# Optimization experiments

Hardware: AMD Instinct MI355X
Metric: run time of the kernel (lower is better)

The kernel has to match this reference:

```python
import jax, jax.numpy as jnp
import numpy as np

TAU = 0.5  # temperature from init_kwargs


def _semi_loss(h1, h2):
    # GRACE-style InfoNCE: -log( e^{sim(i,i')/tau} / (sum_refl + sum_between - e^{sim(i,i)/tau}) )
    n1 = h1 / jnp.linalg.norm(h1, axis=1, keepdims=True)
    n2 = h2 / jnp.linalg.norm(h2, axis=1, keepdims=True)
    refl = jnp.exp((n1 @ n1.T) / TAU)   # [N, N]
    betw = jnp.exp((n1 @ n2.T) / TAU)   # [N, N]
    denom = refl.sum(axis=1) + betw.sum(axis=1) - jnp.diagonal(refl)
    return -jnp.log(jnp.diagonal(betw) / denom)


def _contrast(h1, h2):
    # forward_v1 with batch_size=0 (batched path is mathematically identical)
    return (0.5 * (_semi_loss(h1, h2) + _semi_loss(h2, h1))).mean()


def _proj(z, Wa, ba, Wb, bb):
    # fc_b(elu(fc_a(z))); torch Linear: y = x @ W.T + b
    return jax.nn.elu(z @ Wa.T + ba) @ Wb.T + bb


def setup_inputs() -> dict:
    key = jax.random.key(0)
    ks = jax.random.split(key, 11)
    N, A, B = 8192, 32, 32
    D = A * B
    s = 1.0 / np.sqrt(D)
    inp = {
        'ta': jax.random.normal(ks[0], (N, A, B), dtype=jnp.float32),
        'tb': jax.random.normal(ks[1], (N, A, B), dtype=jnp.float32),
        'W1': jax.random.uniform(ks[2], (D, D), jnp.float32, -s, s),
        'b1': jax.random.uniform(ks[3], (D,), jnp.float32, -s, s),
        'W2': jax.random.uniform(ks[4], (D, D), jnp.float32, -s, s),
        'b2': jax.random.uniform(ks[5], (D,), jnp.float32, -s, s),
        'W3': jax.random.uniform(ks[6], (D, D), jnp.float32, -s, s),
        'b3': jax.random.uniform(ks[7], (D,), jnp.float32, -s, s),
        'W4': jax.random.uniform(ks[8], (D, D), jnp.float32, -s, s),
        'b4': jax.random.uniform(ks[9], (D,), jnp.float32, -s, s),
        'w_r1': jnp.array([0.5], dtype=jnp.float32),
    }
    return inp


def reference(ta, tb, W1, b1, W2, b2, W3, b3, W4, b4, w_r1):
    N = ta.shape[0]
    # row view: [N, A*B]
    z1 = ta.reshape(N, -1)
    z2 = tb.reshape(N, -1)
    loss_row = _contrast(_proj(z1, W1, b1, W2, b2), _proj(z2, W1, b1, W2, b2))
    # column view: permute(0,2,1) then flatten -> [N, B*A]
    z1c = jnp.transpose(ta, (0, 2, 1)).reshape(N, -1)
    z2c = jnp.transpose(tb, (0, 2, 1)).reshape(N, -1)
    loss_col = _contrast(_proj(z1c, W3, b3, W4, b4), _proj(z2c, W3, b3, W4, b4))
    w_row = jnp.clip(w_r1[0], 0.0, 1.0)
    return w_row * loss_row + (1.0 - w_row) * loss_col
```

## Files before the change

kernel.cpp:

```cpp
#include <hip/hip_runtime.h>
#include <stdint.h>


typedef unsigned short u16;
typedef __attribute__((ext_vector_type(8))) __bf16 bf16x8;
typedef __attribute__((ext_vector_type(4))) float f32x4;

#define NS 8192
#define DD 1024

__device__ __forceinline__ float bf2f(u16 u) {
    union { uint32_t i; float f; } v; v.i = ((uint32_t)u) << 16; return v.f;
}
__device__ __forceinline__ u16 f2bf(float f) {
    union { float f; uint32_t i; } v; v.f = f;
    return (u16)((v.i + 0x7FFFu + ((v.i >> 16) & 1u)) >> 16);
}

__device__ __forceinline__ void gload16(const u16* g, u16* l) {
    __builtin_amdgcn_global_load_lds(
        (__attribute__((address_space(1))) void*)(uintptr_t)(g),
        (__attribute__((address_space(3))) void*)(uintptr_t)(l), 16, 0, 0);
}


__global__ __launch_bounds__(256) void conv_f2bf(const float* __restrict__ src,
                                                 u16* __restrict__ dst) {
    int i = (blockIdx.x * 256 + threadIdx.x) * 4;
    float4 v = *(const float4*)(src + i);
    ushort4 o;
    o.x = f2bf(v.x); o.y = f2bf(v.y); o.z = f2bf(v.z); o.w = f2bf(v.w);
    *(ushort4*)(dst + i) = o;
}

__global__ __launch_bounds__(256) void conv_cat(const float* __restrict__ a,
                                                const float* __restrict__ b,
                                                u16* __restrict__ Z) {
    size_t i = (size_t)(blockIdx.x * 256 + threadIdx.x) * 4;
    const size_t half = (size_t)NS * DD;
    const float* s = (i < half) ? (a + i) : (b + (i - half));
    float4 v = *(const float4*)s;
    ushort4 o;
    o.x = f2bf(v.x); o.y = f2bf(v.y); o.z = f2bf(v.z); o.w = f2bf(v.w);
    *(ushort4*)(Z + i) = o;
}

__global__ __launch_bounds__(256) void conv_col(const float* __restrict__ a,
                                                const float* __restrict__ b,
                                                u16* __restrict__ Z) {
    size_t i = (size_t)(blockIdx.x * 256 + threadIdx.x) * 4;
    const size_t half = (size_t)NS * DD;
    const float* src; size_t o;
    if (i < half) { src = a; o = i; } else { src = b; o = i - half; }
    size_t row = o >> 10;
    int j = (int)(o & 1023);
    int aI = j & 31, bI = j >> 5;
    const float* rp = src + (row << 10);
    ushort4 ov;
    ov.x = f2bf(rp[aI * 32 + bI]);
    ov.y = f2bf(rp[(aI + 1) * 32 + bI]);
    ov.z = f2bf(rp[(aI + 2) * 32 + bI]);
    ov.w = f2bf(rp[(aI + 3) * 32 + bI]);
    *(ushort4*)(Z + i) = ov;
}

template <int MODE>
__global__ __launch_bounds__(256) void gemm_bt(const u16* A, const u16* B,
                                               const float* __restrict__ bias,
                                               u16* __restrict__ out) {
    __shared__ alignas(16) u16 As[128 * 32];
    __shared__ alignas(16) u16 Bs[128 * 32];
    const int tid = threadIdx.x;

    const int tm = blockIdx.y, tn = blockIdx.x;
    const size_t tileM = (size_t)tm * 128;
    const size_t tileN = (size_t)tn * 128;

    const int csw = ((tid & 3) ^ ((tid >> 4) & 3)) * 8;
    const u16* gA0 = A + (tileM + (tid >> 2)) * DD + csw;
    const u16* gA1 = gA0 + (size_t)64 * DD;
    const u16* gB0 = B + (tileN + (tid >> 2)) * DD + csw;
    const u16* gB1 = gB0 + (size_t)64 * DD;
    u16* lA0 = &As[tid * 8]; u16* lA1 = lA0 + 2048;
    u16* lB0 = &Bs[tid * 8]; u16* lB1 = lB0 + 2048;

    const int lane = tid & 63;
    const int wv = tid >> 6;
    const int wr = (wv >> 1) << 6;
    const int wc = (wv & 1) << 6;
    const int lr = lane & 15;
    const int lh = lane >> 4;
    const int sw = lh ^ ((lr >> 2) & 3);

    const u16* aBase = &As[(wr + lr) * 32 + sw * 8];
    const u16* bBase = &Bs[(wc + lr) * 32 + sw * 8];

    f32x4 acc[4][4];
#pragma unroll
    for (int i = 0; i < 4; i++)
#pragma unroll
        for (int j = 0; j < 4; j++) acc[i][j] = (f32x4)0.0f;

    for (int k0 = 0; k0 < DD; k0 += 32) {
        gload16(gA0 + k0, lA0);
        gload16(gA1 + k0, lA1);
        gload16(gB0 + k0, lB0);
        gload16(gB1 + k0, lB1);
        __syncthreads();
        bf16x8 af[4], bfr[4];
#pragma unroll
        for (int rt = 0; rt < 4; rt++) af[rt] = *(const bf16x8*)(aBase + rt * 512);
#pragma unroll
        for (int ct = 0; ct < 4; ct++) bfr[ct] = *(const bf16x8*)(bBase + ct * 512);
#pragma unroll
        for (int rt = 0; rt < 4; rt++)
#pragma unroll
            for (int ct = 0; ct < 4; ct++)
                acc[rt][ct] = __builtin_amdgcn_mfma_f32_16x16x32_bf16(
                    af[rt], bfr[ct], acc[rt][ct], 0, 0, 0);
        __syncthreads();
    }

    float bcol[4];
#pragma unroll
    for (int ct = 0; ct < 4; ct++) bcol[ct] = bias[tileN + wc + ct * 16 + lr];
#pragma unroll
    for (int rt = 0; rt < 4; rt++) {
#pragma unroll
        for (int r = 0; r < 4; r++) {
            size_t row = tileM + wr + rt * 16 + lh * 4 + r;
            u16* orow = out + row * DD + tileN + wc + lr;
#pragma unroll
            for (int ct = 0; ct < 4; ct++) {
                float v = acc[rt][ct][r] + bcol[ct];
                if (MODE == 0) v = v > 0.0f ? v : expm1f(v);
                orow[ct * 16] = f2bf(v);
            }
        }
    }
}

__global__ __launch_bounds__(512, 2) void gram256(const u16* __restrict__ H,
                                                  float* __restrict__ S) {
    __shared__ alignas(16) u16 LA[4][256 * 32];
    __shared__ alignas(16) u16 LB[4][256 * 32];
    const int tid = threadIdx.x;

    int x = blockIdx.x, y = blockIdx.y;
    int tm, tn;
    if (y + x < 64) { tm = y;      tn = y + x; }
    else            { tm = 63 - y; tn = x - 1; }

    const size_t rowA = (size_t)tm * 256;
    const size_t rowB = (size_t)tn * 256;

    const int r_lo = tid >> 2;
    const int csw  = ((tid & 3) ^ ((r_lo >> 2) & 3)) * 8;
    const u16* gA0 = H + (rowA + r_lo) * DD + csw;
    const u16* gA1 = H + (rowA + 128 + r_lo) * DD + csw;
    const u16* gB0 = H + (rowB + r_lo) * DD + csw;
    const u16* gB1 = H + (rowB + 128 + r_lo) * DD + csw;
    const int ldst = tid * 8;

    const int lane = tid & 63;
    const int wv = tid >> 6;
    const int wr = (wv >> 2) * 128;
    const int wc = (wv & 3) * 64;
    const int lr = lane & 15;
    const int lh = lane >> 4;
    const int sw = lh ^ ((lr >> 2) & 3);
    const int aoff = (wr + lr) * 32 + sw * 8;
    const int boff = (wc + lr) * 32 + sw * 8;

    f32x4 acc[8][4];
#pragma unroll
    for (int i = 0; i < 8; ++i)
#pragma unroll
        for (int j = 0; j < 4; ++j) acc[i][j] = (f32x4)0.0f;

#pragma unroll
    for (int t = 0; t < 3; ++t) {
        const int k0 = t * 32;
        gload16(gA0 + k0, &LA[t][0] + ldst);
        gload16(gA1 + k0, &LA[t][4096] + ldst);
        gload16(gB0 + k0, &LB[t][0] + ldst);
        gload16(gB1 + k0, &LB[t][4096] + ldst);
    }

    for (int t = 0; t < 32; ++t) {
        if (t < 30)       asm volatile("s_waitcnt vmcnt(8)" ::: "memory");
        else if (t == 30) asm volatile("s_waitcnt vmcnt(4)" ::: "memory");
        else              asm volatile("s_waitcnt vmcnt(0)" ::: "memory");
        __builtin_amdgcn_s_barrier();
        asm volatile("" ::: "memory");

        const int buf = t & 3;
        const u16* la = &LA[buf][0];
        const u16* lb = &LB[buf][0];

        bf16x8 bF[4], aF[8];
#pragma unroll
        for (int i = 0; i < 4; ++i) bF[i] = *(const bf16x8*)(lb + boff + i * 512);
#pragma unroll
        for (int i = 0; i < 8; ++i) aF[i] = *(const bf16x8*)(la + aoff + i * 512);

        if (t < 29) {
            const int nbuf = (t + 3) & 3;
            const int k0n = (t + 3) * 32;
            gload16(gA0 + k0n, &LA[nbuf][0] + ldst);
            gload16(gA1 + k0n, &LA[nbuf][4096] + ldst);
            gload16(gB0 + k0n, &LB[nbuf][0] + ldst);
            gload16(gB1 + k0n, &LB[nbuf][4096] + ldst);
        }

        __builtin_amdgcn_s_setprio(1);
#pragma unroll
        for (int mi = 0; mi < 8; ++mi)
#pragma unroll
            for (int ni = 0; ni < 4; ++ni)
                acc[mi][ni] = __builtin_amdgcn_mfma_f32_16x16x32_bf16(
                    aF[mi], bF[ni], acc[mi][ni], 0, 0, 0);
        __builtin_amdgcn_s_setprio(0);
    }

    const bool offdiag = (tm != tn);
    float colsum[4] = {0.f, 0.f, 0.f, 0.f};
#pragma unroll
    for (int q = 0; q < 8; ++q) {
#pragma unroll
        for (int r = 0; r < 4; ++r) {
            float rs = 0.0f;
#pragma unroll
            for (int ni = 0; ni < 4; ++ni) {
                float e = __expf(2.0f * acc[q][ni][r]);
                rs += e;
                colsum[ni] += e;
            }
            rs += __shfl_xor(rs, 1);
            rs += __shfl_xor(rs, 2);
            rs += __shfl_xor(rs, 4);
            rs += __shfl_xor(rs, 8);
            if (lr == 0) {
                size_t row = rowA + wr + q * 16 + lh * 4 + r;
                atomicAdd(&S[row], rs);
            }
        }
    }
    if (offdiag) {
#pragma unroll
        for (int ni = 0; ni < 4; ++ni) {
            float cs = colsum[ni];
            cs += __shfl_xor(cs, 16);
            cs += __shfl_xor(cs, 32);
            if (lh == 0) {
                size_t col = rowB + wc + ni * 16 + lr;
                atomicAdd(&S[col], cs);
            }
        }
    }
}

__global__ __launch_bounds__(256) void normalize_kernel(u16* M) {
    __shared__ float red[4];
    const int tid = threadIdx.x;
    u16* row = M + ((size_t)blockIdx.x << 10);
    ushort4 v = ((const ushort4*)row)[tid];
    float x0 = bf2f(v.x), x1 = bf2f(v.y), x2 = bf2f(v.z), x3 = bf2f(v.w);
    float s = x0 * x0 + x1 * x1 + x2 * x2 + x3 * x3;
#pragma unroll
    for (int m = 1; m < 64; m <<= 1) s += __shfl_xor(s, m);
    if ((tid & 63) == 0) red[tid >> 6] = s;
    __syncthreads();
    float inv = rsqrtf(red[0] + red[1] + red[2] + red[3]);
    ushort4 o;
    o.x = f2bf(x0 * inv); o.y = f2bf(x1 * inv);
    o.z = f2bf(x2 * inv); o.w = f2bf(x3 * inv);
    ((ushort4*)row)[tid] = o;
}

__global__ __launch_bounds__(256) void diag_kernel(const u16* M, float* g12) {
    __shared__ float red[4];
    const int tid = threadIdx.x;
    const u16* r1 = M + ((size_t)blockIdx.x << 10);
    const u16* r2 = r1 + ((size_t)NS << 10);
    ushort4 a = ((const ushort4*)r1)[tid];
    ushort4 b = ((const ushort4*)r2)[tid];
    float s = bf2f(a.x) * bf2f(b.x) + bf2f(a.y) * bf2f(b.y) +
              bf2f(a.z) * bf2f(b.z) + bf2f(a.w) * bf2f(b.w);
#pragma unroll
    for (int m = 1; m < 64; m <<= 1) s += __shfl_xor(s, m);
    if ((tid & 63) == 0) red[tid >> 6] = s;
    __syncthreads();
    if (tid == 0) g12[blockIdx.x] = red[0] + red[1] + red[2] + red[3];
}

__global__ __launch_bounds__(256) void final_kernel(const float* Sr, const float* Sc,
                                                    const float* gr, const float* gc,
                                                    const float* w_r1, float* out) {
    __shared__ float red[16];
    const float E2 = 7.389056098930650f;
    float a = 0.f, b = 0.f, c = 0.f, d = 0.f;
    for (int i = threadIdx.x; i < 2 * NS; i += 256) {
        a += logf(Sr[i] - E2);
        b += logf(Sc[i] - E2);
    }
    for (int i = threadIdx.x; i < NS; i += 256) {
        c += gr[i];
        d += gc[i];
    }
#pragma unroll
    for (int m = 1; m < 64; m <<= 1) {
        a += __shfl_xor(a, m); b += __shfl_xor(b, m);
        c += __shfl_xor(c, m); d += __shfl_xor(d, m);
    }
    int w = threadIdx.x >> 6;
    if ((threadIdx.x & 63) == 0) {
        red[w] = a; red[4 + w] = b; red[8 + w] = c; red[12 + w] = d;
    }
    __syncthreads();
    if (threadIdx.x == 0) {
        a = red[0] + red[1] + red[2] + red[3];
        b = red[4] + red[5] + red[6] + red[7];
        c = red[8] + red[9] + red[10] + red[11];
        d = red[12] + red[13] + red[14] + red[15];
        float lr = a / (2.0f * NS) - 2.0f * c / NS;
        float lc = b / (2.0f * NS) - 2.0f * d / NS;
        float w0 = w_r1[0];
        w0 = fminf(fmaxf(w0, 0.0f), 1.0f);
        out[0] = w0 * lr + (1.0f - w0) * lc;
    }
}

extern "C" void kernel_launch(void* const* d_in, const int* in_sizes, int n_in,
                              void* d_out, int out_size, void* d_ws, size_t ws_size,
                              hipStream_t stream) {
    const float* ta = (const float*)d_in[0];
    const float* tb = (const float*)d_in[1];
    const float* W1 = (const float*)d_in[2];
    const float* b1 = (const float*)d_in[3];
    const float* W2 = (const float*)d_in[4];
    const float* b2 = (const float*)d_in[5];
    const float* W3 = (const float*)d_in[6];
    const float* b3 = (const float*)d_in[7];
    const float* W4 = (const float*)d_in[8];
    const float* b4 = (const float*)d_in[9];
    const float* wr = (const float*)d_in[10];
    float* out = (float*)d_out;

    char* p = (char*)d_ws;
    const size_t MAT = (size_t)2 * NS * DD * sizeof(u16);
    u16* Z = (u16*)p;  p += MAT;
    u16* T = (u16*)p;  p += MAT;
    u16* H = (u16*)p;  p += MAT;
    u16* Wb = (u16*)p; p += (size_t)4 * DD * DD * sizeof(u16);
    float* Sr = (float*)p;  p += 2 * NS * sizeof(float);
    float* Sc = (float*)p;  p += 2 * NS * sizeof(float);
    float* gr = (float*)p;  p += NS * sizeof(float);
    float* gc = (float*)p;  p += NS * sizeof(float);

    u16* Wb1 = Wb;
    u16* Wb2 = Wb + (size_t)DD * DD;
    u16* Wb3 = Wb + (size_t)2 * DD * DD;
    u16* Wb4 = Wb + (size_t)3 * DD * DD;

    conv_f2bf<<<1024, 256, 0, stream>>>(W1, Wb1);
    conv_f2bf<<<1024, 256, 0, stream>>>(W2, Wb2);
    conv_f2bf<<<1024, 256, 0, stream>>>(W3, Wb3);
    conv_f2bf<<<1024, 256, 0, stream>>>(W4, Wb4);
    hipMemsetAsync(Sr, 0, 4 * NS * sizeof(float), stream);

    conv_cat<<<16384, 256, 0, stream>>>(ta, tb, Z);
    gemm_bt<0><<<dim3(8, 128), 256, 0, stream>>>(Z, Wb1, b1, T);
    gemm_bt<1><<<dim3(8, 128), 256, 0, stream>>>(T, Wb2, b2, H);
    normalize_kernel<<<16384, 256, 0, stream>>>(H);
    diag_kernel<<<8192, 256, 0, stream>>>(H, gr);
    gram256<<<dim3(65, 32), 512, 0, stream>>>(H, Sr);

    conv_col<<<16384, 256, 0, stream>>>(ta, tb, Z);
    gemm_bt<0><<<dim3(8, 128), 256, 0, stream>>>(Z, Wb3, b3, T);
    gemm_bt<1><<<dim3(8, 128), 256, 0, stream>>>(T, Wb4, b4, H);
    normalize_kernel<<<16384, 256, 0, stream>>>(H);
    diag_kernel<<<8192, 256, 0, stream>>>(H, gc);
    gram256<<<dim3(65, 32), 512, 0, stream>>>(H, Sc);

    final_kernel<<<1, 256, 0, stream>>>(Sr, Sc, gr, gc, wr, out);
}
```

Before: 1.180 ms.

## Restructure gram kernel main loop into 8-wave ping-pong with BK=64 double buffer

Replaces the 4-stage BK=32 LDS ring in the Gram kernel with a two-buffer BK=64 scheme. Each K step is split into four quadrant MFMA phases, and the next tile's global-to-LDS loads are interleaved between them under explicit barriers, waitcnts and sched_barriers. The goal is to overlap memory traffic with MFMA work in a ping-pong schedule and to halve the number of loop iterations. In exchange it adds many more barriers per iteration and changes the LDS swizzle, which risks bank conflicts or stalls if the waitcnt accounting is off.

```diff
diff --git a/kernel.cpp b/kernel.cpp
--- a/kernel.cpp
+++ b/kernel.cpp
@@ -22,6 +22,10 @@
         (__attribute__((address_space(1))) void*)(uintptr_t)(g),
         (__attribute__((address_space(3))) void*)(uintptr_t)(l), 16, 0, 0);
 }
+
+#define BARRIER() do { asm volatile("" ::: "memory"); \
+    __builtin_amdgcn_s_barrier(); \
+    asm volatile("" ::: "memory"); } while (0)
 
 
 __global__ __launch_bounds__(256) void conv_f2bf(const float* __restrict__ src,
@@ -142,35 +146,35 @@
 
 __global__ __launch_bounds__(512, 2) void gram256(const u16* __restrict__ H,
                                                   float* __restrict__ S) {
-    __shared__ alignas(16) u16 LA[4][256 * 32];
-    __shared__ alignas(16) u16 LB[4][256 * 32];
+    __shared__ alignas(16) u16 L[2][32768];
     const int tid = threadIdx.x;
 
     int x = blockIdx.x, y = blockIdx.y;
     int tm, tn;
     if (y + x < 64) { tm = y;      tn = y + x; }
     else            { tm = 63 - y; tn = x - 1; }
-
     const size_t rowA = (size_t)tm * 256;
     const size_t rowB = (size_t)tn * 256;
 
-    const int r_lo = tid >> 2;
-    const int csw  = ((tid & 3) ^ ((r_lo >> 2) & 3)) * 8;
-    const u16* gA0 = H + (rowA + r_lo) * DD + csw;
-    const u16* gA1 = H + (rowA + 128 + r_lo) * DD + csw;
-    const u16* gB0 = H + (rowB + r_lo) * DD + csw;
-    const u16* gB1 = H + (rowB + 128 + r_lo) * DD + csw;
-    const int ldst = tid * 8;
-
-    const int lane = tid & 63;
-    const int wv = tid >> 6;
+    const int gcol = (((tid & 7) ^ (((tid >> 5) & 1) << 1)) << 3);
+    const u16* gAlo = H + (rowA + (tid >> 3)) * DD + gcol;
+    const u16* gAhi = gAlo + (size_t)128 * DD;
+    const u16* gBlo = H + (rowB + (tid >> 3)) * DD + gcol;
+    const u16* gBhi = gBlo + (size_t)128 * DD;
+    const int sdst = tid * 8;
+
+#define STG(g, nb, off, ko) do { \
+    gload16((g) + (ko), (nb) + (off) + sdst); \
+    gload16((g) + (ko) + (size_t)64 * DD, (nb) + (off) + 4096 + sdst); } while (0)
+
+    const int lane = tid & 63, wv = tid >> 6;
     const int wr = (wv >> 2) * 128;
     const int wc = (wv & 3) * 64;
     const int lr = lane & 15;
     const int lh = lane >> 4;
-    const int sw = lh ^ ((lr >> 2) & 3);
-    const int aoff = (wr + lr) * 32 + sw * 8;
-    const int boff = (wc + lr) * 32 + sw * 8;
+    const int lh2 = lh ^ (((lr >> 2) & 1) << 1);
+    const int aRd = (wr + lr) * 64 + lh2 * 8;
+    const int bRd = 16384 + (wc + lr) * 64 + lh2 * 8;
 
     f32x4 acc[8][4];
 #pragma unroll
@@ -178,50 +182,113 @@
 #pragma unroll
         for (int j = 0; j < 4; ++j) acc[i][j] = (f32x4)0.0f;
 
-#pragma unroll
-    for (int t = 0; t < 3; ++t) {
-        const int k0 = t * 32;
-        gload16(gA0 + k0, &LA[t][0] + ldst);
-        gload16(gA1 + k0, &LA[t][4096] + ldst);
-        gload16(gB0 + k0, &LB[t][0] + ldst);
-        gload16(gB1 + k0, &LB[t][4096] + ldst);
-    }
-
-    for (int t = 0; t < 32; ++t) {
-        if (t < 30)       asm volatile("s_waitcnt vmcnt(8)" ::: "memory");
-        else if (t == 30) asm volatile("s_waitcnt vmcnt(4)" ::: "memory");
-        else              asm volatile("s_waitcnt vmcnt(0)" ::: "memory");
-        __builtin_amdgcn_s_barrier();
-        asm volatile("" ::: "memory");
-
-        const int buf = t & 3;
-        const u16* la = &LA[buf][0];
-        const u16* lb = &LB[buf][0];
-
-        bf16x8 bF[4], aF[8];
-#pragma unroll
-        for (int i = 0; i < 4; ++i) bF[i] = *(const bf16x8*)(lb + boff + i * 512);
-#pragma unroll
-        for (int i = 0; i < 8; ++i) aF[i] = *(const bf16x8*)(la + aoff + i * 512);
-
-        if (t < 29) {
-            const int nbuf = (t + 3) & 3;
-            const int k0n = (t + 3) * 32;
-            gload16(gA0 + k0n, &LA[nbuf][0] + ldst);
-            gload16(gA1 + k0n, &LA[nbuf][4096] + ldst);
-            gload16(gB0 + k0n, &LB[nbuf][0] + ldst);
-            gload16(gB1 + k0n, &LB[nbuf][4096] + ldst);
+    {
+        u16* nb = &L[0][0];
+        STG(gBlo, nb, 16384, 0);
+        STG(gBhi, nb, 24576, 0);
+        STG(gAlo, nb, 0,     0);
+        STG(gAhi, nb, 8192,  0);
+    }
+    asm volatile("s_waitcnt vmcnt(2)" ::: "memory");
+    BARRIER();
+
+    for (int t = 0; t < 16; ++t) {
+        const u16* lp = &L[t & 1][0];
+        u16* nb = &L[(t & 1) ^ 1][0];
+        const int ko = (t + 1) * 64;
+        bf16x8 aF[8], bF0[4], bF1[4];
+
+#pragma unroll
+        for (int q = 0; q < 4; ++q)
+#pragma unroll
+            for (int kk = 0; kk < 2; ++kk)
+                aF[q * 2 + kk] = *(const bf16x8*)(lp + aRd + q * 1024 + kk * 32);
+#pragma unroll
+        for (int n = 0; n < 2; ++n)
+#pragma unroll
+            for (int kk = 0; kk < 2; ++kk)
+                bF0[n * 2 + kk] = *(const bf16x8*)(lp + bRd + n * 1024 + kk * 32);
+        if (t < 15) STG(gBlo, nb, 16384, ko);
+        BARRIER();
+        asm volatile("s_waitcnt lgkmcnt(0)" ::: "memory");
+        __builtin_amdgcn_sched_barrier(0);
+        __builtin_amdgcn_s_setprio(1);
+#pragma unroll
+        for (int q = 0; q < 4; ++q)
+#pragma unroll
+            for (int n = 0; n < 2; ++n)
+#pragma unroll
+                for (int kk = 0; kk < 2; ++kk)
+                    acc[q][n] = __builtin_amdgcn_mfma_f32_16x16x32_bf16(
+                        aF[q * 2 + kk], bF0[n * 2 + kk], acc[q][n], 0, 0, 0);
+        __builtin_amdgcn_s_setprio(0);
+        BARRIER();
+
+#pragma unroll
+        for (int n = 0; n < 2; ++n)
+#pragma unroll
+            for (int kk = 0; kk < 2; ++kk)
+                bF1[n * 2 + kk] = *(const bf16x8*)(lp + bRd + (2 + n) * 1024 + kk * 32);
+        if (t < 15) {
+            STG(gBhi, nb, 24576, ko);
+            asm volatile("s_waitcnt vmcnt(4)" ::: "memory");
+        } else {
+            asm volatile("s_waitcnt vmcnt(0)" ::: "memory");
         }
-
+        BARRIER();
+        asm volatile("s_waitcnt lgkmcnt(0)" ::: "memory");
+        __builtin_amdgcn_sched_barrier(0);
         __builtin_amdgcn_s_setprio(1);
 #pragma unroll
-        for (int mi = 0; mi < 8; ++mi)
-#pragma unroll
-            for (int ni = 0; ni < 4; ++ni)
-                acc[mi][ni] = __builtin_amdgcn_mfma_f32_16x16x32_bf16(
-                    aF[mi], bF[ni], acc[mi][ni], 0, 0, 0);
+        for (int q = 0; q < 4; ++q)
+#pragma unroll
+            for (int n = 0; n < 2; ++n)
+#pragma unroll
+                for (int kk = 0; kk < 2; ++kk)
+                    acc[q][2 + n] = __builtin_amdgcn_mfma_f32_16x16x32_bf16(
+                        aF[q * 2 + kk], bF1[n * 2 + kk], acc[q][2 + n], 0, 0, 0);
         __builtin_amdgcn_s_setprio(0);
-    }
+        BARRIER();
+
+#pragma unroll
+        for (int q = 0; q < 4; ++q)
+#pragma unroll
+            for (int kk = 0; kk < 2; ++kk)
+                aF[q * 2 + kk] = *(const bf16x8*)(lp + aRd + 4096 + q * 1024 + kk * 32);
+        if (t < 15) STG(gAlo, nb, 0, ko);
+        BARRIER();
+        asm volatile("s_waitcnt lgkmcnt(0)" ::: "memory");
+        __builtin_amdgcn_sched_barrier(0);
+        __builtin_amdgcn_s_setprio(1);
+#pragma unroll
+        for (int q = 0; q < 4; ++q)
+#pragma unroll
+            for (int n = 0; n < 2; ++n)
+#pragma unroll
+                for (int kk = 0; kk < 2; ++kk)
+                    acc[4 + q][2 + n] = __builtin_amdgcn_mfma_f32_16x16x32_bf16(
+                        aF[q * 2 + kk], bF1[n * 2 + kk], acc[4 + q][2 + n], 0, 0, 0);
+        __builtin_amdgcn_s_setprio(0);
+        BARRIER();
+
+        if (t < 15) {
+            STG(gAhi, nb, 8192, ko);
+            asm volatile("s_waitcnt vmcnt(2)" ::: "memory");
+        }
+        BARRIER();
+        __builtin_amdgcn_s_setprio(1);
+#pragma unroll
+        for (int q = 0; q < 4; ++q)
+#pragma unroll
+            for (int n = 0; n < 2; ++n)
+#pragma unroll
+                for (int kk = 0; kk < 2; ++kk)
+                    acc[4 + q][n] = __builtin_amdgcn_mfma_f32_16x16x32_bf16(
+                        aF[q * 2 + kk], bF0[n * 2 + kk], acc[4 + q][n], 0, 0, 0);
+        __builtin_amdgcn_s_setprio(0);
+        BARRIER();
+    }
+#undef STG
 
     const bool offdiag = (tm != tn);
     float colsum[4] = {0.f, 0.f, 0.f, 0.f};
```

New measurement: 1.258 ms. +6.6%, slower.

## Use 32x32 MFMA in gram kernel and fuse row/column gram launches

Applied to the files above, without the earlier changes.

The Gram-matrix kernel switches from 16x16x32 to 32x32x16 bf16 MFMA tiles, with a new LDS fragment addressing and reduction layout. The column-view projection now writes into a separate buffer so both views' Gram computations run in a single launch with twice the grid. This aims to raise MFMA throughput, cut LDS reads per FLOP, and remove a serialized launch and tail. It assumes the column sums buffer sits directly after the row buffer.

```diff
diff --git a/kernel.cpp b/kernel.cpp
--- a/kernel.cpp
+++ b/kernel.cpp
@@ -5,6 +5,7 @@
 typedef unsigned short u16;
 typedef __attribute__((ext_vector_type(8))) __bf16 bf16x8;
 typedef __attribute__((ext_vector_type(4))) float f32x4;
+typedef __attribute__((ext_vector_type(16))) float f32x16;
 
 #define NS 8192
 #define DD 1024
@@ -140,13 +141,17 @@
     }
 }
 
-__global__ __launch_bounds__(512, 2) void gram256(const u16* __restrict__ H,
-                                                  float* __restrict__ S) {
+__global__ __launch_bounds__(512, 2) void gram256(const u16* __restrict__ Hr,
+                                                  const u16* __restrict__ Hc,
+                                                  float* __restrict__ Sbase) {
     __shared__ alignas(16) u16 LA[4][256 * 32];
     __shared__ alignas(16) u16 LB[4][256 * 32];
     const int tid = threadIdx.x;
 
-    int x = blockIdx.x, y = blockIdx.y;
+    const int view = (int)blockIdx.y >> 5;
+    const u16* H = view ? Hc : Hr;
+    float* S = Sbase + view * 2 * NS;
+    const int x = blockIdx.x, y = (int)blockIdx.y & 31;
     int tm, tn;
     if (y + x < 64) { tm = y;      tn = y + x; }
     else            { tm = 63 - y; tn = x - 1; }
@@ -166,17 +171,19 @@
     const int wv = tid >> 6;
     const int wr = (wv >> 2) * 128;
     const int wc = (wv & 3) * 64;
-    const int lr = lane & 15;
-    const int lh = lane >> 4;
-    const int sw = lh ^ ((lr >> 2) & 3);
-    const int aoff = (wr + lr) * 32 + sw * 8;
-    const int boff = (wc + lr) * 32 + sw * 8;
-
-    f32x4 acc[8][4];
-#pragma unroll
-    for (int i = 0; i < 8; ++i)
-#pragma unroll
-        for (int j = 0; j < 4; ++j) acc[i][j] = (f32x4)0.0f;
+    const int c31 = lane & 31;
+    const int hi  = lane >> 5;
+    const int q4  = (c31 >> 2) & 3;
+    const int o0  = (hi ^ q4) * 8;
+    const int o1  = ((hi ^ q4) ^ 2) * 8;
+    const int aBase = (wr + c31) * 32;
+    const int bBase = (wc + c31) * 32;
+
+    f32x16 acc[4][2];
+#pragma unroll
+    for (int i = 0; i < 4; ++i)
+#pragma unroll
+        for (int j = 0; j < 2; ++j) acc[i][j] = (f32x16)0.0f;
 
 #pragma unroll
     for (int t = 0; t < 3; ++t) {
@@ -193,16 +200,6 @@
         else              asm volatile("s_waitcnt vmcnt(0)" ::: "memory");
         __builtin_amdgcn_s_barrier();
         asm volatile("" ::: "memory");
-
-        const int buf = t & 3;
-        const u16* la = &LA[buf][0];
-        const u16* lb = &LB[buf][0];
-
-        bf16x8 bF[4], aF[8];
-#pragma unroll
-        for (int i = 0; i < 4; ++i) bF[i] = *(const bf16x8*)(lb + boff + i * 512);
-#pragma unroll
-        for (int i = 0; i < 8; ++i) aF[i] = *(const bf16x8*)(la + aoff + i * 512);
 
         if (t < 29) {
             const int nbuf = (t + 3) & 3;
@@ -213,47 +210,65 @@
             gload16(gB1 + k0n, &LB[nbuf][4096] + ldst);
         }
 
+        const int buf = t & 3;
+        const u16* la = &LA[buf][0];
+        const u16* lb = &LB[buf][0];
+
+        bf16x8 aF[4][2], bF[2][2];
+#pragma unroll
+        for (int nt = 0; nt < 2; ++nt) {
+            bF[nt][0] = *(const bf16x8*)(lb + bBase + nt * 1024 + o0);
+            bF[nt][1] = *(const bf16x8*)(lb + bBase + nt * 1024 + o1);
+        }
+#pragma unroll
+        for (int mt = 0; mt < 4; ++mt) {
+            aF[mt][0] = *(const bf16x8*)(la + aBase + mt * 1024 + o0);
+            aF[mt][1] = *(const bf16x8*)(la + aBase + mt * 1024 + o1);
+        }
+
         __builtin_amdgcn_s_setprio(1);
 #pragma unroll
-        for (int mi = 0; mi < 8; ++mi)
-#pragma unroll
-            for (int ni = 0; ni < 4; ++ni)
-                acc[mi][ni] = __builtin_amdgcn_mfma_f32_16x16x32_bf16(
-                    aF[mi], bF[ni], acc[mi][ni], 0, 0, 0);
+        for (int mt = 0; mt < 4; ++mt)
+#pragma unroll
+            for (int nt = 0; nt < 2; ++nt)
+#pragma unroll
+                for (int kk = 0; kk < 2; ++kk)
+                    acc[mt][nt] = __builtin_amdgcn_mfma_f32_32x32x16_bf16(
+                        aF[mt][kk], bF[nt][kk], acc[mt][nt], 0, 0, 0);
         __builtin_amdgcn_s_setprio(0);
     }
 
     const bool offdiag = (tm != tn);
-    float colsum[4] = {0.f, 0.f, 0.f, 0.f};
-#pragma unroll
-    for (int q = 0; q < 8; ++q) {
-#pragma unroll
-        for (int r = 0; r < 4; ++r) {
+    float csum[2] = {0.f, 0.f};
+#pragma unroll
+    for (int mt = 0; mt < 4; ++mt) {
+#pragma unroll
+        for (int j = 0; j < 16; ++j) {
             float rs = 0.0f;
 #pragma unroll
-            for (int ni = 0; ni < 4; ++ni) {
-                float e = __expf(2.0f * acc[q][ni][r]);
+            for (int nt = 0; nt < 2; ++nt) {
+                float e = __expf(2.0f * acc[mt][nt][j]);
                 rs += e;
-                colsum[ni] += e;
+                csum[nt] += e;
             }
             rs += __shfl_xor(rs, 1);
             rs += __shfl_xor(rs, 2);
             rs += __shfl_xor(rs, 4);
             rs += __shfl_xor(rs, 8);
-            if (lr == 0) {
-                size_t row = rowA + wr + q * 16 + lh * 4 + r;
+            rs += __shfl_xor(rs, 16);
+            if (c31 == 0) {
+                size_t row = rowA + wr + mt * 32 + (j & 3) + 8 * (j >> 2) + 4 * hi;
                 atomicAdd(&S[row], rs);
             }
         }
     }
     if (offdiag) {
 #pragma unroll
-        for (int ni = 0; ni < 4; ++ni) {
-            float cs = colsum[ni];
-            cs += __shfl_xor(cs, 16);
+        for (int nt = 0; nt < 2; ++nt) {
+            float cs = csum[nt];
             cs += __shfl_xor(cs, 32);
-            if (lh == 0) {
-                size_t col = rowB + wc + ni * 16 + lr;
+            if (hi == 0) {
+                size_t col = rowB + wc + nt * 32 + c31;
                 atomicAdd(&S[col], cs);
             }
         }
@@ -374,14 +389,14 @@
     gemm_bt<1><<<dim3(8, 128), 256, 0, stream>>>(T, Wb2, b2, H);
     normalize_kernel<<<16384, 256, 0, stream>>>(H);
     diag_kernel<<<8192, 256, 0, stream>>>(H, gr);
-    gram256<<<dim3(65, 32), 512, 0, stream>>>(H, Sr);
 
     conv_col<<<16384, 256, 0, stream>>>(ta, tb, Z);
     gemm_bt<0><<<dim3(8, 128), 256, 0, stream>>>(Z, Wb3, b3, T);
-    gemm_bt<1><<<dim3(8, 128), 256, 0, stream>>>(T, Wb4, b4, H);
-    normalize_kernel<<<16384, 256, 0, stream>>>(H);
-    diag_kernel<<<8192, 256, 0, stream>>>(H, gc);
-    gram256<<<dim3(65, 32), 512, 0, stream>>>(H, Sc);
+    gemm_bt<1><<<dim3(8, 128), 256, 0, stream>>>(T, Wb4, b4, Z);
+    normalize_kernel<<<16384, 256, 0, stream>>>(Z);
+    diag_kernel<<<8192, 256, 0, stream>>>(Z, gc);
+
+    gram256<<<dim3(65, 64), 512, 0, stream>>>(H, Z, Sr);
 
     final_kernel<<<1, 256, 0, stream>>>(Sr, Sc, gr, gc, wr, out);
 }
```

Result: slower. 1.399 ms (+18.6%).

## Fuse normalize with diagonal, batch weight conversions, merge both gram launches

Applied to the files above, without the earlier changes.

The four weight-conversion launches become a single kernel that picks its source matrix by block index. The normalize and diagonal kernels are merged so each block normalizes a matching pair of rows and computes their dot product in one pass, which avoids re-reading H. The column-view projection now writes into the spare Z buffer, so one gram256 launch with a doubled grid covers both views and gives the GPU more blocks per wave. In exchange, Sc must sit directly after Sr in the workspace, and the diagonal is computed from rounded bf16 values as before.

```diff
diff --git a/kernel.cpp b/kernel.cpp
--- a/kernel.cpp
+++ b/kernel.cpp
@@ -24,13 +24,19 @@
 }
 
 
-__global__ __launch_bounds__(256) void conv_f2bf(const float* __restrict__ src,
-                                                 u16* __restrict__ dst) {
-    int i = (blockIdx.x * 256 + threadIdx.x) * 4;
-    float4 v = *(const float4*)(src + i);
+__global__ __launch_bounds__(256) void conv_f2bf4(const float* __restrict__ W1,
+                                                  const float* __restrict__ W2,
+                                                  const float* __restrict__ W3,
+                                                  const float* __restrict__ W4,
+                                                  u16* __restrict__ dst) {
+    const int b = blockIdx.x;
+    const float* src = (b < 1024) ? W1 : (b < 2048) ? W2 : (b < 3072) ? W3 : W4;
+    const size_t so = ((size_t)(b & 1023) << 10) + threadIdx.x * 4;
+    const size_t dо = ((size_t)b << 10) + threadIdx.x * 4;
+    float4 v = *(const float4*)(src + so);
     ushort4 o;
     o.x = f2bf(v.x); o.y = f2bf(v.y); o.z = f2bf(v.z); o.w = f2bf(v.w);
-    *(ushort4*)(dst + i) = o;
+    *(ushort4*)(dst + dо) = o;
 }
 
 __global__ __launch_bounds__(256) void conv_cat(const float* __restrict__ a,
@@ -140,13 +146,17 @@
     }
 }
 
-__global__ __launch_bounds__(512, 2) void gram256(const u16* __restrict__ H,
-                                                  float* __restrict__ S) {
+__global__ __launch_bounds__(512, 2) void gram256(const u16* __restrict__ Hr,
+                                                  const u16* __restrict__ Hc,
+                                                  float* __restrict__ Sbase) {
     __shared__ alignas(16) u16 LA[4][256 * 32];
     __shared__ alignas(16) u16 LB[4][256 * 32];
     const int tid = threadIdx.x;
 
-    int x = blockIdx.x, y = blockIdx.y;
+    const int view = (int)blockIdx.y >> 5;
+    const u16* H = view ? Hc : Hr;
+    float* S = Sbase + view * 2 * NS;
+    int x = blockIdx.x, y = (int)blockIdx.y & 31;
     int tm, tn;
     if (y + x < 64) { tm = y;      tn = y + x; }
     else            { tm = 63 - y; tn = x - 1; }
@@ -260,38 +270,41 @@
     }
 }
 
-__global__ __launch_bounds__(256) void normalize_kernel(u16* M) {
-    __shared__ float red[4];
+__global__ __launch_bounds__(256) void normdiag_kernel(u16* M, float* g12) {
+    __shared__ float red[12];
     const int tid = threadIdx.x;
-    u16* row = M + ((size_t)blockIdx.x << 10);
-    ushort4 v = ((const ushort4*)row)[tid];
-    float x0 = bf2f(v.x), x1 = bf2f(v.y), x2 = bf2f(v.z), x3 = bf2f(v.w);
-    float s = x0 * x0 + x1 * x1 + x2 * x2 + x3 * x3;
-#pragma unroll
-    for (int m = 1; m < 64; m <<= 1) s += __shfl_xor(s, m);
-    if ((tid & 63) == 0) red[tid >> 6] = s;
+    u16* r1 = M + ((size_t)blockIdx.x << 10);
+    u16* r2 = r1 + ((size_t)NS << 10);
+    ushort4 va = ((const ushort4*)r1)[tid];
+    ushort4 vb = ((const ushort4*)r2)[tid];
+    float a0 = bf2f(va.x), a1 = bf2f(va.y), a2 = bf2f(va.z), a3 = bf2f(va.w);
+    float b0 = bf2f(vb.x), b1 = bf2f(vb.y), b2 = bf2f(vb.z), b3 = bf2f(vb.w);
+    float s1 = a0 * a0 + a1 * a1 + a2 * a2 + a3 * a3;
+    float s2 = b0 * b0 + b1 * b1 + b2 * b2 + b3 * b3;
+#pragma unroll
+    for (int m = 1; m < 64; m <<= 1) {
+        s1 += __shfl_xor(s1, m);
+        s2 += __shfl_xor(s2, m);
+    }
+    const int w = tid >> 6;
+    if ((tid & 63) == 0) { red[w] = s1; red[4 + w] = s2; }
     __syncthreads();
-    float inv = rsqrtf(red[0] + red[1] + red[2] + red[3]);
-    ushort4 o;
-    o.x = f2bf(x0 * inv); o.y = f2bf(x1 * inv);
-    o.z = f2bf(x2 * inv); o.w = f2bf(x3 * inv);
-    ((ushort4*)row)[tid] = o;
-}
-
-__global__ __launch_bounds__(256) void diag_kernel(const u16* M, float* g12) {
-    __shared__ float red[4];
-    const int tid = threadIdx.x;
-    const u16* r1 = M + ((size_t)blockIdx.x << 10);
-    const u16* r2 = r1 + ((size_t)NS << 10);
-    ushort4 a = ((const ushort4*)r1)[tid];
-    ushort4 b = ((const ushort4*)r2)[tid];
-    float s = bf2f(a.x) * bf2f(b.x) + bf2f(a.y) * bf2f(b.y) +
-              bf2f(a.z) * bf2f(b.z) + bf2f(a.w) * bf2f(b.w);
-#pragma unroll
-    for (int m = 1; m < 64; m <<= 1) s += __shfl_xor(s, m);
-    if ((tid & 63) == 0) red[tid >> 6] = s;
+    float inv1 = rsqrtf(red[0] + red[1] + red[2] + red[3]);
+    float inv2 = rsqrtf(red[4] + red[5] + red[6] + red[7]);
+    ushort4 oa, ob;
+    oa.x = f2bf(a0 * inv1); oa.y = f2bf(a1 * inv1);
+    oa.z = f2bf(a2 * inv1); oa.w = f2bf(a3 * inv1);
+    ob.x = f2bf(b0 * inv2); ob.y = f2bf(b1 * inv2);
+    ob.z = f2bf(b2 * inv2); ob.w = f2bf(b3 * inv2);
+    ((ushort4*)r1)[tid] = oa;
+    ((ushort4*)r2)[tid] = ob;
+    float d = bf2f(oa.x) * bf2f(ob.x) + bf2f(oa.y) * bf2f(ob.y) +
+              bf2f(oa.z) * bf2f(ob.z) + bf2f(oa.w) * bf2f(ob.w);
+#pragma unroll
+    for (int m = 1; m < 64; m <<= 1) d += __shfl_xor(d, m);
+    if ((tid & 63) == 0) red[8 + w] = d;
     __syncthreads();
-    if (tid == 0) g12[blockIdx.x] = red[0] + red[1] + red[2] + red[3];
+    if (tid == 0) g12[blockIdx.x] = red[8] + red[9] + red[10] + red[11];
 }
 
 __global__ __launch_bounds__(256) void final_kernel(const float* Sr, const float* Sc,
@@ -363,25 +376,20 @@
     u16* Wb3 = Wb + (size_t)2 * DD * DD;
     u16* Wb4 = Wb + (size_t)3 * DD * DD;
 
-    conv_f2bf<<<1024, 256, 0, stream>>>(W1, Wb1);
-    conv_f2bf<<<1024, 256, 0, stream>>>(W2, Wb2);
-    conv_f2bf<<<1024, 256, 0, stream>>>(W3, Wb3);
-    conv_f2bf<<<1024, 256, 0, stream>>>(W4, Wb4);
+    conv_f2bf4<<<4096, 256, 0, stream>>>(W1, W2, W3, W4, Wb);
     hipMemsetAsync(Sr, 0, 4 * NS * sizeof(float), stream);
 
     conv_cat<<<16384, 256, 0, stream>>>(ta, tb, Z);
     gemm_bt<0><<<dim3(8, 128), 256, 0, stream>>>(Z, Wb1, b1, T);
     gemm_bt<1><<<dim3(8, 128), 256, 0, stream>>>(T, Wb2, b2, H);
-    normalize_kernel<<<16384, 256, 0, stream>>>(H);
-    diag_kernel<<<8192, 256, 0, stream>>>(H, gr);
-    gram256<<<dim3(65, 32), 512, 0, stream>>>(H, Sr);
+    normdiag_kernel<<<8192, 256, 0, stream>>>(H, gr);
 
     conv_col<<<16384, 256, 0, stream>>>(ta, tb, Z);
     gemm_bt<0><<<dim3(8, 128), 256, 0, stream>>>(Z, Wb3, b3, T);
-    gemm_bt<1><<<dim3(8, 128), 256, 0, stream>>>(T, Wb4, b4, H);
-    normalize_kernel<<<16384, 256, 0, stream>>>(H);
-    diag_kernel<<<8192, 256, 0, stream>>>(H, gc);
-    gram256<<<dim3(65, 32), 512, 0, stream>>>(H, Sc);
+    gemm_bt<1><<<dim3(8, 128), 256, 0, stream>>>(T, Wb4, b4, Z);
+    normdiag_kernel<<<8192, 256, 0, stream>>>(Z, gc);
+
+    gram256<<<dim3(65, 64), 512, 0, stream>>>(H, Z, Sr);
 
     final_kernel<<<1, 256, 0, stream>>>(Sr, Sc, gr, gc, wr, out);
 }
```

Result: faster. 1.124 ms (-4.8%).
